# Optimization experiments

Hardware: AMD Instinct MI355X
Metric: run time of the kernel (lower is better)

## Reference

```python
import jax, jax.numpy as jnp
from jax import lax
import numpy as np

NUM_FILTERS = 24
NUM_BASIS = 31
GAMMA = 0.5


def setup_inputs() -> dict:
    key = jax.random.key(0)
    k1, k2, k3, k4 = jax.random.split(key, 4)
    B, H, W = 8, 512, 512
    u = jax.random.uniform(k1, (B, 1, H, W), dtype=jnp.float32)
    f = jax.random.uniform(k2, (B, 1, H, W), dtype=jnp.float32)
    filters = jax.random.normal(k3, (NUM_FILTERS, 1, 5, 5), dtype=jnp.float32) * 0.08
    # each RBFInfluence: mu = linspace(-1,1,31) (identical init per filter), weights = randn*0.1
    mu = jnp.tile(jnp.linspace(-1.0, 1.0, NUM_BASIS, dtype=jnp.float32)[None, :], (NUM_FILTERS, 1))
    weights = jax.random.normal(k4, (NUM_FILTERS, NUM_BASIS), dtype=jnp.float32) * 0.1
    lambda_param = jnp.float32(0.15)
    return {"u": u, "f": f, "filters": filters, "mu": mu, "weights": weights,
            "lambda_param": lambda_param}


def _avg_pool3(x):
    # F.avg_pool2d(kernel=3, stride=1, padding=1), count_include_pad=True -> always /9
    s = lax.reduce_window(x, 0.0, lax.add, (1, 1, 3, 3), (1, 1, 1, 1),
                          [(0, 0), (0, 0), (1, 1), (1, 1)])
    return s / 9.0


def reference(u, f, filters, mu, weights, lambda_param):
    u = jnp.clip(u, 1e-4, 1.0)
    f = jnp.clip(f, 1e-4, 1.0)
    dn = ("NCHW", "OIHW", "NCHW")
    # all per-filter 5x5 convs batched as one conv: [B,1,H,W] -> [B,K,H,W]
    conv = lax.conv_general_dilated(u, filters, (1, 1), [(2, 2), (2, 2)], dimension_numbers=dn)
    # RBF influence per filter: phi = sum_j w[c,j] * exp(-(conv - mu[c,j])^2 / (2*gamma^2))
    inv2g2 = 1.0 / (2.0 * GAMMA * GAMMA)
    phi = jnp.zeros_like(conv)
    for j in range(NUM_BASIS):  # small fixed loop; avoids [B,K,H,W,31] intermediate
        d = conv - mu[:, j][None, :, None, None]
        phi = phi + weights[:, j][None, :, None, None] * jnp.exp(-(d * d) * inv2g2)
    # u_sigma / M identical across filter loop iterations in the original -> hoisted
    u_sigma = _avg_pool3(u)  # [B,1,H,W]
    M = jnp.mean(u_sigma) + 0.001
    scaled_phi = (u_sigma / M) * phi  # [B,K,H,W]
    # sum_i conv2d(scaled_phi_i, flip(k_i)) == single conv with [1,K,5,5] kernel
    kT = jnp.transpose(jnp.flip(filters, axis=(2, 3)), (1, 0, 2, 3))  # [1,K,5,5]
    diffusion = lax.conv_general_dilated(scaled_phi, kT, (1, 1), [(2, 2), (2, 2)],
                                         dimension_numbers=dn)  # [B,1,H,W]
    reaction = lambda_param * (u - f) / (u + 0.05)
    return jnp.clip(u - diffusion - reaction, 0.0, 1.0)
```

## Files before the change

### kernel.cpp

```cpp
#include <hip/hip_runtime.h>
#include <hip/hip_fp16.h>
#include <math.h>

#define NBATCH 8
#define HH 512
#define WW 512
#define NF 24
#define NB 31
#define TH 32
#define TW 64
#define SPH (TH + 4)
#define SPW (TW + 4)
#define UH (TH + 8)
#define UW (TW + 8)
#define SU_S 76
#define SP_S 76
#define NTHR 192
#define SP_TASKS 153
#define CV_TASKS 128
#define LUTN 256
#define WS_LO 8
#define WS_SC 40
#define WS_LUT 72
#define WS_PART (WS_LUT + NF * LUTN)
#define WS_REQ ((WS_PART + 1024) * 4)

__device__ __forceinline__ void phi_pair(const float* mu, const float* wts, int c,
                                         float x, float h, float* p0, float* p1) {
    float a = 0.f, b = 0.f;
    for (int j = 0; j < NB; ++j) {
        float m = mu[c * NB + j], w = wts[c * NB + j];
        float d0 = x - m, d1 = x + h - m;
        a += w * __expf(-2.f * d0 * d0);
        b += w * __expf(-2.f * d1 * d1);
    }
    *p0 = a; *p1 = b;
}

__device__ __forceinline__ void filter_range(const float* filt, int c,
                                             float* lo_, float* rng_) {
    float lo = 0.f, hi = 0.f;
    for (int i = 0; i < 25; ++i) {
        float k = filt[c * 25 + i];
        lo += fminf(k, 0.f);
        hi += fmaxf(k, 0.f);
    }
    *lo_ = lo;
    *rng_ = fmaxf(hi - lo, 1e-9f);
}

__global__ __launch_bounds__(256) void pre_kernel(const float* __restrict__ u,
                                                  const float* __restrict__ filt,
                                                  const float* __restrict__ mu,
                                                  const float* __restrict__ wts,
                                                  float* __restrict__ ws, int do_lut) {
    __shared__ float sred[4];
    const int tid = threadIdx.x;
    const int N = NBATCH * HH * WW;
    int stride = gridDim.x * blockDim.x;
    float s = 0.f;
    for (int i = blockIdx.x * blockDim.x + tid; i < N; i += stride) {
        int x = i & (WW - 1);
        int y = (i >> 9) & (HH - 1);
        float v = fminf(fmaxf(u[i], 1e-4f), 1.0f);
        float wy = (y == 0 || y == HH - 1) ? 2.f : 3.f;
        float wx = (x == 0 || x == WW - 1) ? 2.f : 3.f;
        s += v * (wy * wx);
    }
#pragma unroll
    for (int off = 32; off > 0; off >>= 1) s += __shfl_down(s, off, 64);
    if ((tid & 63) == 0) sred[tid >> 6] = s;
    __syncthreads();
    if (tid == 0) ws[WS_PART + blockIdx.x] = sred[0] + sred[1] + sred[2] + sred[3];

    if (do_lut && blockIdx.x < NF) {
        const int c = blockIdx.x;
        float lo, rng;
        filter_range(filt, c, &lo, &rng);
        float h = rng * (1.f / 255.f);
        float p0, p1;
        phi_pair(mu, wts, c, lo + (float)tid * h, h, &p0, &p1);
        unsigned u0 = (unsigned)__half_as_ushort(__float2half(p0));
        unsigned u1 = (unsigned)__half_as_ushort(__float2half(p1));
        ((unsigned*)ws)[WS_LUT + c * LUTN + tid] = u0 | (u1 << 16);
        if (tid == 0) { ws[WS_LO + c] = lo; ws[WS_SC + c] = 255.f / rng; }
    }
}

__device__ __forceinline__ void sp_phase(int pr0, int pc0,
                                         const float (*su)[SU_S], float (*spb)[SP_S],
                                         const unsigned* __restrict__ slc,
                                         float scc, float offc,
                                         const float* __restrict__ fc,
                                         const float (&usg)[4][4]) {
    float acc[4][4] = {{0.f}};
#pragma unroll
    for (int ky = 0; ky < 8; ++ky) {
        float4 a = *(const float4*)&su[pr0 + ky][pc0];
        float4 b = *(const float4*)&su[pr0 + ky][pc0 + 4];
        float t8[8] = {a.x, a.y, a.z, a.w, b.x, b.y, b.z, b.w};
#pragma unroll
        for (int r = 0; r < 4; ++r) {
            if (ky - r < 0 || ky - r > 4) continue;
            const int kyy = ky - r;
#pragma unroll
            for (int dx = 0; dx < 5; ++dx) {
                float w = fc[kyy * 5 + dx];
#pragma unroll
                for (int k = 0; k < 4; ++k)
                    acc[r][k] = fmaf(w, t8[k + dx], acc[r][k]);
            }
        }
    }
#pragma unroll
    for (int r = 0; r < 4; ++r) {
        float o[4];
#pragma unroll
        for (int k = 0; k < 4; ++k) {
            float t = fmaf(acc[r][k], scc, offc);
            t = fminf(fmaxf(t, 0.f), 254.999f);
            int i0 = (int)t;
            float fr = t - (float)i0;
            unsigned pk = slc[i0];
            __half2 hv = *reinterpret_cast<const __half2*>(&pk);
            float2 fv = __half22float2(hv);
            o[k] = fmaf(fr, fv.y - fv.x, fv.x) * usg[r][k];
        }
        *(float4*)&spb[pr0 + r][pc0] = make_float4(o[0], o[1], o[2], o[3]);
    }
}

template <bool WSLUT>
__global__ __launch_bounds__(NTHR) void tnrd_kernel(
    const float* __restrict__ u, const float* __restrict__ f,
    const float* __restrict__ filt, const float* __restrict__ mu,
    const float* __restrict__ wts, const float* __restrict__ lamp,
    const float* __restrict__ ws, float* __restrict__ out)
{
    __shared__ float su[UH][SU_S];
    __shared__ float sp[2][SPH][SP_S];
    __shared__ unsigned slut[2][LUTN];
    __shared__ float swred[3];

    const int tid = threadIdx.x;
    const int bz = blockIdx.z;
    const int oy0 = blockIdx.y * TH;
    const int ox0 = blockIdx.x * TW;
    const float* ub = u + bz * HH * WW;
    const unsigned* lutg = (const unsigned*)ws + WS_LUT;

#pragma unroll
    for (int j = 0; j < (UH * UW) / NTHR; ++j) {
        int i = j * NTHR + tid;
        int uy = i / UW, ux = i - uy * UW;
        int gy = oy0 - 4 + uy, gx = ox0 - 4 + ux;
        float v = 0.f;
        if ((unsigned)gy < (unsigned)HH && (unsigned)gx < (unsigned)WW)
            v = fminf(fmaxf(ub[gy * WW + gx], 1e-4f), 1.0f);
        su[uy][ux] = v;
    }

    if (WSLUT) {
        for (int i = tid; i < 2 * LUTN; i += NTHR) (&slut[0][0])[i] = lutg[i];
    } else {
        for (int c = 0; c < 2; ++c) {
            float lo, rng;
            filter_range(filt, c, &lo, &rng);
            float h = rng * (1.f / 255.f);
            for (int e = tid; e < LUTN; e += NTHR) {
                float p0, p1;
                phi_pair(mu, wts, c, lo + (float)e * h, h, &p0, &p1);
                unsigned u0 = (unsigned)__half_as_ushort(__float2half(p0));
                unsigned u1 = (unsigned)__half_as_ushort(__float2half(p1));
                slut[c][e] = u0 | (u1 << 16);
            }
        }
    }

    {
        float ps = 0.f;
        for (int i = tid; i < 1024; i += NTHR) ps += ws[WS_PART + i];
#pragma unroll
        for (int off = 32; off > 0; off >>= 1) ps += __shfl_down(ps, off, 64);
        if ((tid & 63) == 0) swred[tid >> 6] = ps;
    }
    __syncthreads();

    const float tot = swred[0] + swred[1] + swred[2];
    const float Mv = tot * (1.0f / (9.0f * NBATCH * HH * WW)) + 0.001f;
    const float inv9M = (1.f / 9.f) / Mv;

    const int qr = tid / 17, qc = tid - qr * 17;
    const int pr0 = qr * 4, pc0 = qc * 4;
    const int tr = tid >> 4, tc = tid & 15;
    const int or0 = tr * 4, oc0 = tc * 4;

    float usg[4][4];
    if (tid < SP_TASKS) {
        float hr[6][4];
#pragma unroll
        for (int j = 0; j < 6; ++j) {
            float4 a = *(const float4*)&su[pr0 + 1 + j][pc0];
            float4 b = *(const float4*)&su[pr0 + 1 + j][pc0 + 4];
            float t8[8] = {a.x, a.y, a.z, a.w, b.x, b.y, b.z, b.w};
#pragma unroll
            for (int k = 0; k < 4; ++k)
                hr[j][k] = t8[k + 1] + t8[k + 2] + t8[k + 3];
        }
#pragma unroll
        for (int r = 0; r < 4; ++r) {
            int gy = oy0 - 2 + pr0 + r;
            bool ry = (unsigned)gy < (unsigned)HH;
#pragma unroll
            for (int k = 0; k < 4; ++k) {
                int gx = ox0 - 2 + pc0 + k;
                bool ok = ry && (unsigned)gx < (unsigned)WW;
                usg[r][k] = ok ? (hr[r][k] + hr[r + 1][k] + hr[r + 2][k]) * inv9M : 0.f;
            }
        }
    }

    if (tid < SP_TASKS) {
        float lo, scc;
        if (WSLUT) { lo = ws[WS_LO]; scc = ws[WS_SC]; }
        else { float rng; filter_range(filt, 0, &lo, &rng); scc = 255.f / rng; }
        sp_phase(pr0, pc0, su, sp[0], &slut[0][0], scc, -lo * scc, filt, usg);
    }
    __syncthreads();

    float dif[4][4] = {{0.f}};

    for (int c = 0; c < NF; ++c) {
        if (c + 1 < NF && tid < SP_TASKS) {
            int cn = c + 1;
            float lo, scc;
            if (WSLUT) { lo = ws[WS_LO + cn]; scc = ws[WS_SC + cn]; }
            else { float rng; filter_range(filt, cn, &lo, &rng); scc = 255.f / rng; }
            sp_phase(pr0, pc0, su, sp[cn & 1], &slut[cn & 1][0],
                     scc, -lo * scc, filt + cn * 25, usg);
        }

        if (tid < CV_TASKS) {
            const float* fc = filt + c * 25;
            const float (*spc)[SP_S] = sp[c & 1];
#pragma unroll
            for (int s = 0; s < 8; ++s) {
                float4 a = *(const float4*)&spc[or0 + s][oc0];
                float4 b = *(const float4*)&spc[or0 + s][oc0 + 4];
                float t8[8] = {a.x, a.y, a.z, a.w, b.x, b.y, b.z, b.w};
#pragma unroll
                for (int r = 0; r < 4; ++r) {
                    if (s - r < 0 || s - r > 4) continue;
                    const int dy = s - r;
#pragma unroll
                    for (int dx = 0; dx < 5; ++dx) {
                        float w = fc[(4 - dy) * 5 + (4 - dx)];
#pragma unroll
                        for (int k = 0; k < 4; ++k)
                            dif[r][k] = fmaf(w, t8[k + dx], dif[r][k]);
                    }
                }
            }
        } else if (c + 2 < NF) {
            int t = tid - CV_TASKS;
            int cn = c + 2;
            if (WSLUT) {
#pragma unroll
                for (int j = 0; j < 4; ++j)
                    slut[cn & 1][t + 64 * j] = lutg[cn * LUTN + t + 64 * j];
            } else {
                float lo, rng;
                filter_range(filt, cn, &lo, &rng);
                float h = rng * (1.f / 255.f);
#pragma unroll
                for (int j = 0; j < 4; ++j) {
                    int e = t + 64 * j;
                    float p0, p1;
                    phi_pair(mu, wts, cn, lo + (float)e * h, h, &p0, &p1);
                    unsigned u0 = (unsigned)__half_as_ushort(__float2half(p0));
                    unsigned u1 = (unsigned)__half_as_ushort(__float2half(p1));
                    slut[cn & 1][e] = u0 | (u1 << 16);
                }
            }
        }

        if (c + 1 < NF) __syncthreads();
    }

    if (tid < CV_TASKS) {
        const float lam = lamp[0];
        const float* fb = f + bz * HH * WW;
        float* ob = out + bz * HH * WW;
#pragma unroll
        for (int r = 0; r < 4; ++r) {
            int gy = oy0 + or0 + r;
            int gx = ox0 + oc0;
            float4 uv4 = *(const float4*)&su[or0 + r + 4][oc0 + 4];
            float4 fv4 = *(const float4*)&fb[gy * WW + gx];
            float uu[4] = {uv4.x, uv4.y, uv4.z, uv4.w};
            float ff[4] = {fv4.x, fv4.y, fv4.z, fv4.w};
            float o[4];
#pragma unroll
            for (int k = 0; k < 4; ++k) {
                float uv = uu[k];
                float fv = fminf(fmaxf(ff[k], 1e-4f), 1.0f);
                float reac = lam * (uv - fv) / (uv + 0.05f);
                o[k] = fminf(fmaxf(uv - dif[r][k] - reac, 0.f), 1.f);
            }
            *(float4*)&ob[gy * WW + gx] = make_float4(o[0], o[1], o[2], o[3]);
        }
    }
}

extern "C" void kernel_launch(void* const* d_in, const int* in_sizes, int n_in,
                              void* d_out, int out_size, void* d_ws, size_t ws_size,
                              hipStream_t stream) {
    const float* u = (const float*)d_in[0];
    const float* f = (const float*)d_in[1];
    const float* filt = (const float*)d_in[2];
    const float* mu = (const float*)d_in[3];
    const float* wts = (const float*)d_in[4];
    const float* lam = (const float*)d_in[5];
    float* ws = (float*)d_ws;
    float* out = (float*)d_out;

    const bool use_ws = ws_size >= (size_t)WS_REQ;
    pre_kernel<<<1024, 256, 0, stream>>>(u, filt, mu, wts, ws, use_ws ? 1 : 0);
    dim3 grid(WW / TW, HH / TH, NBATCH);
    if (use_ws)
        tnrd_kernel<true><<<grid, NTHR, 0, stream>>>(u, f, filt, mu, wts, lam, ws, out);
    else
        tnrd_kernel<false><<<grid, NTHR, 0, stream>>>(u, f, filt, mu, wts, lam, ws, out);
}
```

Baseline: 218.8 us.

## Split tile into per-wave strips with wave-local pipeline, no block barriers

Restructures the main loop so each of the two waves owns a 16-row strip and computes its own scaled-phi buffer and LUT, synchronising only within the wave through an LDS waitcnt and wave barrier instead of block-wide __syncthreads per filter. The avg-pool scaling map is precomputed once into shared memory, and the phi buffer uses an XOR column swizzle to reduce bank conflicts. Block size drops to 128 threads with launch bounds allowing two blocks per CU. The cost is redundant halo computation of phi rows between strips (20 rows per 16-row strip) and more shared memory per block.

```diff
diff --git a/kernel.cpp b/kernel.cpp
--- a/kernel.cpp
+++ b/kernel.cpp
@@ -9,21 +9,30 @@
 #define NB 31
 #define TH 32
 #define TW 64
-#define SPH (TH + 4)
-#define SPW (TW + 4)
-#define UH (TH + 8)
-#define UW (TW + 8)
+#define STRIP 16
+#define UH 40
+#define UW 72
 #define SU_S 76
-#define SP_S 76
-#define NTHR 192
-#define SP_TASKS 153
-#define CV_TASKS 128
+#define UGH 36
+#define UG_S 76
+#define SPH 20
+#define SP_S 72
+#define NTHR 128
 #define LUTN 256
 #define WS_LO 8
 #define WS_SC 40
 #define WS_LUT 72
 #define WS_PART (WS_LUT + NF * LUTN)
 #define WS_REQ ((WS_PART + 1024) * 4)
+
+__device__ __forceinline__ void wave_lds_fence() {
+    asm volatile("s_waitcnt lgkmcnt(0)" ::: "memory");
+    __builtin_amdgcn_wave_barrier();
+}
+
+__device__ __forceinline__ int sp_col(int r, int c) {
+    return (c < 64) ? (c ^ (((r >> 2) & 3) << 3)) : c;
+}
 
 __device__ __forceinline__ void phi_pair(const float* mu, const float* wts, int c,
                                          float x, float h, float* p0, float* p1) {
@@ -87,71 +96,29 @@
     }
 }
 
-__device__ __forceinline__ void sp_phase(int pr0, int pc0,
-                                         const float (*su)[SU_S], float (*spb)[SP_S],
-                                         const unsigned* __restrict__ slc,
-                                         float scc, float offc,
-                                         const float* __restrict__ fc,
-                                         const float (&usg)[4][4]) {
-    float acc[4][4] = {{0.f}};
-#pragma unroll
-    for (int ky = 0; ky < 8; ++ky) {
-        float4 a = *(const float4*)&su[pr0 + ky][pc0];
-        float4 b = *(const float4*)&su[pr0 + ky][pc0 + 4];
-        float t8[8] = {a.x, a.y, a.z, a.w, b.x, b.y, b.z, b.w};
-#pragma unroll
-        for (int r = 0; r < 4; ++r) {
-            if (ky - r < 0 || ky - r > 4) continue;
-            const int kyy = ky - r;
-#pragma unroll
-            for (int dx = 0; dx < 5; ++dx) {
-                float w = fc[kyy * 5 + dx];
-#pragma unroll
-                for (int k = 0; k < 4; ++k)
-                    acc[r][k] = fmaf(w, t8[k + dx], acc[r][k]);
-            }
-        }
-    }
-#pragma unroll
-    for (int r = 0; r < 4; ++r) {
-        float o[4];
-#pragma unroll
-        for (int k = 0; k < 4; ++k) {
-            float t = fmaf(acc[r][k], scc, offc);
-            t = fminf(fmaxf(t, 0.f), 254.999f);
-            int i0 = (int)t;
-            float fr = t - (float)i0;
-            unsigned pk = slc[i0];
-            __half2 hv = *reinterpret_cast<const __half2*>(&pk);
-            float2 fv = __half22float2(hv);
-            o[k] = fmaf(fr, fv.y - fv.x, fv.x) * usg[r][k];
-        }
-        *(float4*)&spb[pr0 + r][pc0] = make_float4(o[0], o[1], o[2], o[3]);
-    }
-}
-
 template <bool WSLUT>
-__global__ __launch_bounds__(NTHR) void tnrd_kernel(
+__global__ __launch_bounds__(NTHR, 2) void tnrd_kernel(
     const float* __restrict__ u, const float* __restrict__ f,
     const float* __restrict__ filt, const float* __restrict__ mu,
     const float* __restrict__ wts, const float* __restrict__ lamp,
     const float* __restrict__ ws, float* __restrict__ out)
 {
     __shared__ float su[UH][SU_S];
-    __shared__ float sp[2][SPH][SP_S];
-    __shared__ unsigned slut[2][LUTN];
-    __shared__ float swred[3];
+    __shared__ float ug[UGH][UG_S];
+    __shared__ float spb[2][SPH][SP_S];
+    __shared__ unsigned slut[2][2][LUTN];
+    __shared__ float sred[2];
 
     const int tid = threadIdx.x;
+    const int w = tid >> 6;
+    const int lane = tid & 63;
     const int bz = blockIdx.z;
     const int oy0 = blockIdx.y * TH;
     const int ox0 = blockIdx.x * TW;
     const float* ub = u + bz * HH * WW;
     const unsigned* lutg = (const unsigned*)ws + WS_LUT;
 
-#pragma unroll
-    for (int j = 0; j < (UH * UW) / NTHR; ++j) {
-        int i = j * NTHR + tid;
+    for (int i = tid; i < UH * UW; i += NTHR) {
         int uy = i / UW, ux = i - uy * UW;
         int gy = oy0 - 4 + uy, gx = ox0 - 4 + ux;
         float v = 0.f;
@@ -160,142 +127,157 @@
         su[uy][ux] = v;
     }
 
+    {
+        float ps = 0.f;
+#pragma unroll
+        for (int j = 0; j < 1024 / NTHR; ++j) ps += ws[WS_PART + j * NTHR + tid];
+#pragma unroll
+        for (int off = 32; off > 0; off >>= 1) ps += __shfl_down(ps, off, 64);
+        if (lane == 0) sred[w] = ps;
+    }
+
     if (WSLUT) {
-        for (int i = tid; i < 2 * LUTN; i += NTHR) (&slut[0][0])[i] = lutg[i];
-    } else {
-        for (int c = 0; c < 2; ++c) {
-            float lo, rng;
-            filter_range(filt, c, &lo, &rng);
+        ((uint4*)&slut[w][0][0])[lane] = ((const uint4*)lutg)[lane];
+    }
+    __syncthreads();
+
+    const float tot = sred[0] + sred[1];
+    const float Mv = tot * (1.0f / (9.0f * NBATCH * HH * WW)) + 0.001f;
+    const float inv9M = (1.f / 9.f) / Mv;
+
+    for (int i = tid; i < UGH * 17; i += NTHR) {
+        int r = i / 17, t = i - r * 17;
+        int c0 = 4 * t;
+        float s4[4] = {0.f, 0.f, 0.f, 0.f};
+#pragma unroll
+        for (int dy = 0; dy < 3; ++dy) {
+            float4 a = *(const float4*)&su[r + 1 + dy][c0];
+            float4 b = *(const float4*)&su[r + 1 + dy][c0 + 4];
+            float t8[8] = {a.x, a.y, a.z, a.w, b.x, b.y, b.z, b.w};
+#pragma unroll
+            for (int k = 0; k < 4; ++k) s4[k] += t8[k + 1] + t8[k + 2] + t8[k + 3];
+        }
+        int gy = oy0 - 2 + r;
+        bool ry = (unsigned)gy < (unsigned)HH;
+        float o[4];
+#pragma unroll
+        for (int k = 0; k < 4; ++k) {
+            int gx = ox0 - 2 + c0 + k;
+            o[k] = (ry && (unsigned)gx < (unsigned)WW) ? s4[k] * inv9M : 0.f;
+        }
+        *(float4*)&ug[r][c0] = make_float4(o[0], o[1], o[2], o[3]);
+    }
+    __syncthreads();
+
+    float dif[4][4] = {{0.f}};
+    const int or0 = 4 * (lane >> 4);
+    const int oc0 = 4 * (lane & 15);
+    const int wy = w * STRIP;
+    float (*spw)[SP_S] = spb[w];
+
+    for (int c = 0; c < NF; ++c) {
+        const float* fc = filt + c * 25;
+        float lo, scc;
+        uint4 nlut;
+        const bool havepre = WSLUT && (c + 1 < NF);
+        if (havepre) nlut = ((const uint4*)(lutg + (c + 1) * LUTN))[lane];
+        if (WSLUT) {
+            lo = ws[WS_LO + c]; scc = ws[WS_SC + c];
+        } else {
+            float rng; filter_range(filt, c, &lo, &rng); scc = 255.f / rng;
             float h = rng * (1.f / 255.f);
-            for (int e = tid; e < LUTN; e += NTHR) {
+            for (int e = lane; e < LUTN; e += 64) {
                 float p0, p1;
                 phi_pair(mu, wts, c, lo + (float)e * h, h, &p0, &p1);
                 unsigned u0 = (unsigned)__half_as_ushort(__float2half(p0));
                 unsigned u1 = (unsigned)__half_as_ushort(__float2half(p1));
-                slut[c][e] = u0 | (u1 << 16);
+                slut[w][c & 1][e] = u0 | (u1 << 16);
             }
         }
-    }
-
-    {
-        float ps = 0.f;
-        for (int i = tid; i < 1024; i += NTHR) ps += ws[WS_PART + i];
-#pragma unroll
-        for (int off = 32; off > 0; off >>= 1) ps += __shfl_down(ps, off, 64);
-        if ((tid & 63) == 0) swred[tid >> 6] = ps;
-    }
-    __syncthreads();
-
-    const float tot = swred[0] + swred[1] + swred[2];
-    const float Mv = tot * (1.0f / (9.0f * NBATCH * HH * WW)) + 0.001f;
-    const float inv9M = (1.f / 9.f) / Mv;
-
-    const int qr = tid / 17, qc = tid - qr * 17;
-    const int pr0 = qr * 4, pc0 = qc * 4;
-    const int tr = tid >> 4, tc = tid & 15;
-    const int or0 = tr * 4, oc0 = tc * 4;
-
-    float usg[4][4];
-    if (tid < SP_TASKS) {
-        float hr[6][4];
-#pragma unroll
-        for (int j = 0; j < 6; ++j) {
-            float4 a = *(const float4*)&su[pr0 + 1 + j][pc0];
-            float4 b = *(const float4*)&su[pr0 + 1 + j][pc0 + 4];
-            float t8[8] = {a.x, a.y, a.z, a.w, b.x, b.y, b.z, b.w};
-#pragma unroll
-            for (int k = 0; k < 4; ++k)
-                hr[j][k] = t8[k + 1] + t8[k + 2] + t8[k + 3];
-        }
-#pragma unroll
-        for (int r = 0; r < 4; ++r) {
-            int gy = oy0 - 2 + pr0 + r;
-            bool ry = (unsigned)gy < (unsigned)HH;
-#pragma unroll
-            for (int k = 0; k < 4; ++k) {
-                int gx = ox0 - 2 + pc0 + k;
-                bool ok = ry && (unsigned)gx < (unsigned)WW;
-                usg[r][k] = ok ? (hr[r][k] + hr[r + 1][k] + hr[r + 2][k]) * inv9M : 0.f;
-            }
-        }
-    }
-
-    if (tid < SP_TASKS) {
-        float lo, scc;
-        if (WSLUT) { lo = ws[WS_LO]; scc = ws[WS_SC]; }
-        else { float rng; filter_range(filt, 0, &lo, &rng); scc = 255.f / rng; }
-        sp_phase(pr0, pc0, su, sp[0], &slut[0][0], scc, -lo * scc, filt, usg);
-    }
-    __syncthreads();
-
-    float dif[4][4] = {{0.f}};
-
-    for (int c = 0; c < NF; ++c) {
-        if (c + 1 < NF && tid < SP_TASKS) {
-            int cn = c + 1;
-            float lo, scc;
-            if (WSLUT) { lo = ws[WS_LO + cn]; scc = ws[WS_SC + cn]; }
-            else { float rng; filter_range(filt, cn, &lo, &rng); scc = 255.f / rng; }
-            sp_phase(pr0, pc0, su, sp[cn & 1], &slut[cn & 1][0],
-                     scc, -lo * scc, filt + cn * 25, usg);
-        }
-
-        if (tid < CV_TASKS) {
-            const float* fc = filt + c * 25;
-            const float (*spc)[SP_S] = sp[c & 1];
-#pragma unroll
-            for (int s = 0; s < 8; ++s) {
-                float4 a = *(const float4*)&spc[or0 + s][oc0];
-                float4 b = *(const float4*)&spc[or0 + s][oc0 + 4];
-                float t8[8] = {a.x, a.y, a.z, a.w, b.x, b.y, b.z, b.w};
-#pragma unroll
-                for (int r = 0; r < 4; ++r) {
-                    if (s - r < 0 || s - r > 4) continue;
-                    const int dy = s - r;
-#pragma unroll
-                    for (int dx = 0; dx < 5; ++dx) {
-                        float w = fc[(4 - dy) * 5 + (4 - dx)];
-#pragma unroll
-                        for (int k = 0; k < 4; ++k)
-                            dif[r][k] = fmaf(w, t8[k + dx], dif[r][k]);
+        const float offc = -lo * scc;
+        const unsigned* sl = &slut[w][c & 1][0];
+        wave_lds_fence();
+
+#pragma unroll
+        for (int p = 0; p < 3; ++p) {
+            int task = p * 64 + lane;
+            if (task < 170) {
+                int tr = task / 17, tc2 = task - tr * 17;
+                int sr0 = 2 * tr, sc0 = 4 * tc2;
+                float acc[2][4] = {{0.f}};
+#pragma unroll
+                for (int ky = 0; ky < 6; ++ky) {
+                    float4 a = *(const float4*)&su[wy + sr0 + ky][sc0];
+                    float4 b = *(const float4*)&su[wy + sr0 + ky][sc0 + 4];
+                    float t8[8] = {a.x, a.y, a.z, a.w, b.x, b.y, b.z, b.w};
+#pragma unroll
+                    for (int r = 0; r < 2; ++r) {
+                        int kyy = ky - r;
+                        if (kyy < 0 || kyy > 4) continue;
+#pragma unroll
+                        for (int dx = 0; dx < 5; ++dx) {
+                            float wgt = fc[kyy * 5 + dx];
+#pragma unroll
+                            for (int k = 0; k < 4; ++k)
+                                acc[r][k] = fmaf(wgt, t8[k + dx], acc[r][k]);
+                        }
                     }
                 }
-            }
-        } else if (c + 2 < NF) {
-            int t = tid - CV_TASKS;
-            int cn = c + 2;
-            if (WSLUT) {
-#pragma unroll
-                for (int j = 0; j < 4; ++j)
-                    slut[cn & 1][t + 64 * j] = lutg[cn * LUTN + t + 64 * j];
-            } else {
-                float lo, rng;
-                filter_range(filt, cn, &lo, &rng);
-                float h = rng * (1.f / 255.f);
-#pragma unroll
-                for (int j = 0; j < 4; ++j) {
-                    int e = t + 64 * j;
-                    float p0, p1;
-                    phi_pair(mu, wts, cn, lo + (float)e * h, h, &p0, &p1);
-                    unsigned u0 = (unsigned)__half_as_ushort(__float2half(p0));
-                    unsigned u1 = (unsigned)__half_as_ushort(__float2half(p1));
-                    slut[cn & 1][e] = u0 | (u1 << 16);
+#pragma unroll
+                for (int r = 0; r < 2; ++r) {
+                    float4 uu = *(const float4*)&ug[wy + sr0 + r][sc0];
+                    float uu4[4] = {uu.x, uu.y, uu.z, uu.w};
+                    float o[4];
+#pragma unroll
+                    for (int k = 0; k < 4; ++k) {
+                        float t = fmaf(acc[r][k], scc, offc);
+                        t = fminf(fmaxf(t, 0.f), 254.999f);
+                        int i0 = (int)t;
+                        float fr = t - (float)i0;
+                        unsigned pk = sl[i0];
+                        __half2 hv = *reinterpret_cast<const __half2*>(&pk);
+                        float2 fv = __half22float2(hv);
+                        o[k] = fmaf(fr, fv.y - fv.x, fv.x) * uu4[k];
+                    }
+                    *(float4*)&spw[sr0 + r][sp_col(sr0 + r, sc0)] =
+                        make_float4(o[0], o[1], o[2], o[3]);
                 }
             }
         }
-
-        if (c + 1 < NF) __syncthreads();
-    }
-
-    if (tid < CV_TASKS) {
+        wave_lds_fence();
+
+#pragma unroll
+        for (int s = 0; s < 8; ++s) {
+            int rr = or0 + s;
+            float4 a = *(const float4*)&spw[rr][sp_col(rr, oc0)];
+            float4 b = *(const float4*)&spw[rr][sp_col(rr, oc0 + 4)];
+            float t8[8] = {a.x, a.y, a.z, a.w, b.x, b.y, b.z, b.w};
+#pragma unroll
+            for (int r = 0; r < 4; ++r) {
+                int dy = s - r;
+                if (dy < 0 || dy > 4) continue;
+#pragma unroll
+                for (int dx = 0; dx < 5; ++dx) {
+                    float wgt = fc[(4 - dy) * 5 + (4 - dx)];
+#pragma unroll
+                    for (int k = 0; k < 4; ++k)
+                        dif[r][k] = fmaf(wgt, t8[k + dx], dif[r][k]);
+                }
+            }
+        }
+
+        if (havepre) ((uint4*)&slut[w][(c + 1) & 1][0])[lane] = nlut;
+    }
+
+    {
         const float lam = lamp[0];
         const float* fb = f + bz * HH * WW;
         float* ob = out + bz * HH * WW;
 #pragma unroll
         for (int r = 0; r < 4; ++r) {
-            int gy = oy0 + or0 + r;
+            int gy = oy0 + wy + or0 + r;
             int gx = ox0 + oc0;
-            float4 uv4 = *(const float4*)&su[or0 + r + 4][oc0 + 4];
+            float4 uv4 = *(const float4*)&su[wy + or0 + r + 4][oc0 + 4];
             float4 fv4 = *(const float4*)&fb[gy * WW + gx];
             float uu[4] = {uv4.x, uv4.y, uv4.z, uv4.w};
             float ff[4] = {fv4.x, fv4.y, fv4.z, fv4.w};
```

Measured after the change: 211.1 us. 1.04x faster.
